# Kernel tuning notes

Hardware: AMD Instinct MI355X
Metric: run time of the kernel (lower is better)

Reference implementation:

```python
import jax, jax.numpy as jnp
import numpy as np

N_LEVELS = 16
F_PER = 2
LOG2_HASH = 19
HASH_MASK = np.uint32(2 ** LOG2_HASH - 1)
BASE_RES = 16.0
FINEST_RES = 512.0
B_GROWTH = float(np.exp((np.log(FINEST_RES) - np.log(BASE_RES)) / (N_LEVELS - 1)))
PI = float(np.pi)
BOX_MIN = np.array([0.0, -PI, 0.5 * PI, -0.85 * PI], dtype=np.float32)
BOX_MAX = np.array([PI, PI, 0.85 * PI, -0.5 * PI], dtype=np.float32)
PRIMES = np.array([1, 2654435761, 805459861, 3674653429], dtype=np.uint32)
OFFSETS = np.array([[i, j, k, l] for i in (0, 1) for j in (0, 1)
                    for k in (0, 1) for l in (0, 1)], dtype=np.int32)  # (16,4)

BATCH = 131072


def setup_inputs() -> dict:
    key = jax.random.key(0)
    ks = jax.random.split(key, 16)
    bmin, bmax = jnp.asarray(BOX_MIN), jnp.asarray(BOX_MAX)
    u = jax.random.uniform(ks[0], (BATCH, 4), dtype=jnp.float32)
    x = bmin + u * (bmax - bmin)  # points inside the box
    tables = jax.random.uniform(ks[1], (N_LEVELS, 2 ** LOG2_HASH, F_PER),
                                minval=-1e-4, maxval=1e-4, dtype=jnp.float32)

    def lin(k, fi, fo):
        s = 1.0 / np.sqrt(fi)
        k1, k2 = jax.random.split(k)
        W = jax.random.uniform(k1, (fi, fo), minval=-s, maxval=s, dtype=jnp.float32)
        b = jax.random.uniform(k2, (fo,), minval=-s, maxval=s, dtype=jnp.float32)
        return W, b

    W1, b1 = lin(ks[2], 5, 512)
    W2, b2 = lin(ks[3], 512, 512)
    W3, b3 = lin(ks[4], 512, 512)
    W4, b4 = lin(ks[5], 512, 512)
    W5, b5 = lin(ks[6], 512, 512)
    W6, b6 = lin(ks[7], 512, 16)
    return dict(x=x, tables=tables, W1=W1, b1=b1, W2=W2, b2=b2, W3=W3, b3=b3,
                W4=W4, b4=b4, W5=W5, b5=b5, W6=W6, b6=b6)


def _forward(x, tables, W1, b1, W2, b2, W3, b3, W4, b4, W5, b5, W6, b6):
    bmin, bmax = jnp.asarray(BOX_MIN), jnp.asarray(BOX_MAX)
    primes = jnp.asarray(PRIMES)            # (4,) uint32
    offsets = jnp.asarray(OFFSETS)          # (16,4) int32
    B = x.shape[0]

    xc = jnp.clip(x, bmin, bmax)
    keep_mask = jnp.all(x == xc, axis=-1)   # (B,)

    resolutions = jnp.floor(BASE_RES * (B_GROWTH ** jnp.arange(N_LEVELS, dtype=jnp.float32)))

    def level_fn(_, lev):
        table, res = lev                     # table: (2^19, 2), res: scalar
        grid = (bmax - bmin) / res           # (4,)
        bl = jnp.floor((xc - bmin) / grid).astype(jnp.int32)      # (B,4) bottom-left voxel
        verts = (bl[:, None, :] + offsets[None]).astype(jnp.uint32)  # (B,16,4)
        h = verts * primes                   # uint32 wraparound multiply
        h = h[..., 0] ^ h[..., 1] ^ h[..., 2] ^ h[..., 3]
        idx = (h & HASH_MASK).astype(jnp.int32)                   # (B,16)
        emb = table[idx]                     # (B,16,2) gather
        # weight MLP on [resolution, x]
        feat = jnp.concatenate([jnp.broadcast_to(res, (B, 1)).astype(x.dtype), x], axis=1)  # (B,5)
        h1 = jax.nn.relu(feat @ W1 + b1)
        h2 = jax.nn.relu(h1 @ W2 + b2)
        h3 = jax.nn.relu(h2 @ W3 + b3)
        h4 = jax.nn.relu(h3 @ W4 + b4)
        h5 = jax.nn.relu(h4 @ W5 + b5)
        w = jax.nn.softmax(h5 @ W6 + b6, axis=1)                  # (B,16)
        out = jnp.einsum('bv,bvf->bf', w, emb)                    # (B,2)
        return None, out

    _, outs = jax.lax.scan(level_fn, None, (tables, resolutions))  # (L,B,2)
    out = jnp.moveaxis(outs, 0, 1).reshape(B, N_LEVELS * F_PER)    # (B,32)
    return out, keep_mask


def reference(x, tables, W1, b1, W2, b2, W3, b3, W4, b4, W5, b5, W6, b6):
    return _forward(x, tables, W1, b1, W2, b2, W3, b3, W4, b4, W5, b5, W6, b6)
```

## Files before the change

### kernel.cpp

```cpp
#include <hip/hip_runtime.h>
#include <stdint.h>

typedef unsigned int uint32;
typedef unsigned short u16;
typedef unsigned char u8;
typedef long long i64;
typedef unsigned long long u64;
typedef __attribute__((ext_vector_type(4))) float f32x4;

#define HASH_BITS 19
#define TABLE_SZ (1u << HASH_BITS)
#define HMASK (TABLE_SZ - 1u)
#define PI_D 3.141592653589793
#define NPTS 131072
#define NWB4 (4 * 512 * 512)

__device__ __forceinline__ u8 f2fp8(float f) {
    int r = __builtin_amdgcn_cvt_pk_fp8_f32(f, f, 0, false);
    return (u8)(r & 0xFF);
}

__device__ const float g_res[16] = {16.f,20.f,25.f,32.f,40.f,50.f,64.f,80.f,
                                    101.f,128.f,161.f,203.f,256.f,322.f,406.f,512.f};

__global__ void prep_weights(const float* __restrict__ W2, const float* __restrict__ W3,
                             const float* __restrict__ W4, const float* __restrict__ W5,
                             u8* __restrict__ wt8) {
    int pid = blockIdx.x * 256 + threadIdx.x;
    int e = pid * 2;
    if (e < NWB4) {
        int m = e >> 18;
        int rem = e & 262143;
        int n = rem >> 9, k = rem & 511;
        const float* W = (m == 0) ? W2 : (m == 1) ? W3 : (m == 2) ? W4 : W5;
        float v0 = W[k * 512 + n], v1 = W[(k + 1) * 512 + n];
        int g = n >> 4, r = n & 15, kk = k >> 5, kg = (k >> 3) & 3;
        int dst = m * 262144 + g * 8192 + kk * 512 + (kg * 16 + r) * 8 + (k & 7);
        int pk = __builtin_amdgcn_cvt_pk_fp8_f32(v0, v1, 0, false);
        *(u16*)(wt8 + dst) = (u16)(pk & 0xFFFF);
    }
}

__global__ void mask_kernel(const float* __restrict__ x, float* __restrict__ mout, int B) {
    int i = blockIdx.x * 256 + threadIdx.x;
    if (i >= B) return;
    constexpr float bmin[4] = {0.0f, (float)(-PI_D), (float)(0.5 * PI_D), (float)(-0.85 * PI_D)};
    constexpr float bmax[4] = {(float)(PI_D), (float)(PI_D), (float)(0.85 * PI_D), (float)(-0.5 * PI_D)};
    float4 v = ((const float4*)x)[i];
    bool ok = (v.x >= bmin[0]) && (v.x <= bmax[0]) &&
              (v.y >= bmin[1]) && (v.y <= bmax[1]) &&
              (v.z >= bmin[2]) && (v.z <= bmax[2]) &&
              (v.w >= bmin[3]) && (v.w <= bmax[3]);
    mout[i] = ok ? 1.0f : 0.0f;
}

__global__ __launch_bounds__(512, 4)
void fused_mlp(const float* __restrict__ x, const float* __restrict__ tables,
               const float* __restrict__ W1, const float* __restrict__ b1,
               const u8* __restrict__ wt8, const float* __restrict__ W6,
               const float* __restrict__ b2, const float* __restrict__ b3,
               const float* __restrict__ b4, const float* __restrict__ b5,
               const float* __restrict__ b6, float* __restrict__ out, int level) {
    __shared__ u8 act[64 * 512];
    __shared__ u8 w1lds[32 * 512];
    __shared__ u8 w6lds[16 * 512];
    __shared__ float xsh[64 * 4];
    __shared__ float swsh[64 * 17];

    const int tid = threadIdx.x;
    const int lane = tid & 63;
    const int wv = tid >> 6;
    const int ptile = blockIdx.x;
    const float res = g_res[level];
    const int lrow = lane & 15;
    const int kg = lane >> 4;

    if (tid < 256) xsh[tid] = x[(size_t)ptile * 256 + tid];
    {
        int base = tid * 32;
#pragma unroll
        for (int i = 0; i < 32; ++i) {
            int d = base + i;
            int g = d >> 9, w = d & 511, l = w >> 3, j = d & 7;
            int n = g * 16 + (l & 15), k = (l >> 4) * 8 + j;
            float v = (k == 0) ? W1[n] * 512.0f : (k <= 4 ? W1[k * 512 + n] : 0.0f);
            w1lds[d] = f2fp8(v);
        }
    }
    {
        int base = tid * 16;
#pragma unroll
        for (int i = 0; i < 16; ++i) {
            int d = base + i;
            int kk = d >> 9, w = d & 511, l = w >> 3, j = d & 7;
            int n = l & 15, k = kk * 32 + (l >> 4) * 8 + j;
            w6lds[d] = f2fp8(W6[k * 16 + n]);
        }
    }
    __syncthreads();

    f32x4 acc[4][4];
#pragma unroll
    for (int rt = 0; rt < 4; ++rt)
#pragma unroll
        for (int ct = 0; ct < 4; ++ct) acc[rt][ct] = (f32x4){0.f, 0.f, 0.f, 0.f};

    {
        float rs = res * (1.0f / 512.0f);
        i64 bfeat[4];
#pragma unroll
        for (int rt = 0; rt < 4; ++rt) {
            float4 xv = *(const float4*)&xsh[(rt * 16 + lrow) * 4];
            uint32 lo = __builtin_amdgcn_cvt_pk_fp8_f32(rs, xv.x, 0, false);
            lo = __builtin_amdgcn_cvt_pk_fp8_f32(xv.y, xv.z, lo, true);
            uint32 hi = __builtin_amdgcn_cvt_pk_fp8_f32(xv.w, 0.0f, 0, false);
            u64 f = ((u64)hi << 32) | lo;
            bfeat[rt] = (kg == 0) ? (i64)f : (i64)0;
        }
#pragma unroll
        for (int ct = 0; ct < 4; ++ct) {
            i64 a1 = *(const i64*)&w1lds[(wv * 4 + ct) * 512 + lane * 8];
#pragma unroll
            for (int rt = 0; rt < 4; ++rt)
                acc[rt][ct] = __builtin_amdgcn_mfma_f32_16x16x32_fp8_fp8(a1, bfeat[rt], acc[rt][ct], 0, 0, 0);
        }
#pragma unroll
        for (int ct = 0; ct < 4; ++ct) {
            int n0 = wv * 64 + ct * 16 + kg * 4;
            float4 bv = *(const float4*)&b1[n0];
            int u = n0 >> 3, lo2 = n0 & 4;
#pragma unroll
            for (int rt = 0; rt < 4; ++rt) {
                int pt = rt * 16 + lrow;
                float v0 = fmaxf(acc[rt][ct][0] + bv.x, 0.f);
                float v1 = fmaxf(acc[rt][ct][1] + bv.y, 0.f);
                float v2 = fmaxf(acc[rt][ct][2] + bv.z, 0.f);
                float v3 = fmaxf(acc[rt][ct][3] + bv.w, 0.f);
                uint32 wrd = __builtin_amdgcn_cvt_pk_fp8_f32(v0, v1, 0, false);
                wrd = __builtin_amdgcn_cvt_pk_fp8_f32(v2, v3, wrd, true);
                *(uint32*)&act[pt * 512 + ((u ^ (pt & 7)) << 3) + lo2] = wrd;
            }
        }
    }
    __syncthreads();

    for (int ly = 0; ly < 4; ++ly) {
        const float* bias = (ly == 0) ? b2 : (ly == 1) ? b3 : (ly == 2) ? b4 : b5;
#pragma unroll
        for (int rt = 0; rt < 4; ++rt)
#pragma unroll
            for (int ct = 0; ct < 4; ++ct) acc[rt][ct] = (f32x4){0.f, 0.f, 0.f, 0.f};

#pragma unroll
        for (int kk = 0; kk < 16; ++kk) {
            i64 aw[4], ba[4];
#pragma unroll
            for (int ct = 0; ct < 4; ++ct)
                aw[ct] = *(const i64*)&wt8[ly * 262144 + (wv * 4 + ct) * 8192 + kk * 512 + lane * 8];
#pragma unroll
            for (int rt = 0; rt < 4; ++rt) {
                int pt = rt * 16 + lrow;
                ba[rt] = *(const i64*)&act[pt * 512 + (((kk * 4 + kg) ^ (pt & 7)) << 3)];
            }
#pragma unroll
            for (int rt = 0; rt < 4; ++rt)
#pragma unroll
                for (int ct = 0; ct < 4; ++ct)
                    acc[rt][ct] = __builtin_amdgcn_mfma_f32_16x16x32_fp8_fp8(aw[ct], ba[rt], acc[rt][ct], 0, 0, 0);
        }
        __syncthreads();
#pragma unroll
        for (int ct = 0; ct < 4; ++ct) {
            int n0 = wv * 64 + ct * 16 + kg * 4;
            float4 bv = *(const float4*)&bias[n0];
            int u = n0 >> 3, lo2 = n0 & 4;
#pragma unroll
            for (int rt = 0; rt < 4; ++rt) {
                int pt = rt * 16 + lrow;
                float v0 = fmaxf(acc[rt][ct][0] + bv.x, 0.f);
                float v1 = fmaxf(acc[rt][ct][1] + bv.y, 0.f);
                float v2 = fmaxf(acc[rt][ct][2] + bv.z, 0.f);
                float v3 = fmaxf(acc[rt][ct][3] + bv.w, 0.f);
                uint32 wrd = __builtin_amdgcn_cvt_pk_fp8_f32(v0, v1, 0, false);
                wrd = __builtin_amdgcn_cvt_pk_fp8_f32(v2, v3, wrd, true);
                *(uint32*)&act[pt * 512 + ((u ^ (pt & 7)) << 3) + lo2] = wrd;
            }
        }
        __syncthreads();
    }

    if (wv < 4) {
        f32x4 a6 = {0.f, 0.f, 0.f, 0.f};
        const int pt = wv * 16 + lrow;
#pragma unroll
        for (int kk = 0; kk < 16; ++kk) {
            i64 aw = *(const i64*)&w6lds[kk * 512 + lane * 8];
            i64 ba = *(const i64*)&act[pt * 512 + (((kk * 4 + kg) ^ (pt & 7)) << 3)];
            a6 = __builtin_amdgcn_mfma_f32_16x16x32_fp8_fp8(aw, ba, a6, 0, 0, 0);
        }
        int n0 = kg * 4;
        float4 bv = *(const float4*)&b6[n0];
        swsh[pt * 17 + n0 + 0] = a6[0] + bv.x;
        swsh[pt * 17 + n0 + 1] = a6[1] + bv.y;
        swsh[pt * 17 + n0 + 2] = a6[2] + bv.z;
        swsh[pt * 17 + n0 + 3] = a6[3] + bv.w;
    }
    __syncthreads();

    if (tid < 64) {
        float zv[16];
        float m = -1e30f;
#pragma unroll
        for (int j = 0; j < 16; ++j) { zv[j] = swsh[tid * 17 + j]; m = fmaxf(m, zv[j]); }
        float s = 0.f;
#pragma unroll
        for (int j = 0; j < 16; ++j) { zv[j] = expf(zv[j] - m); s += zv[j]; }
        float inv = 1.0f / s;
#pragma unroll
        for (int j = 0; j < 16; ++j) swsh[tid * 17 + j] = zv[j] * inv;
    }
    __syncthreads();

    {
        constexpr float bmin[4] = {0.0f, (float)(-PI_D), (float)(0.5 * PI_D), (float)(-0.85 * PI_D)};
        constexpr float bmax[4] = {(float)(PI_D), (float)(PI_D), (float)(0.85 * PI_D), (float)(-0.5 * PI_D)};
        constexpr uint32 primes[4] = {1u, 2654435761u, 805459861u, 3674653429u};
        const int p = tid >> 3;
        const int pr = tid & 7;
        uint32 ca[4], cb[4];
#pragma unroll
        for (int d = 0; d < 4; ++d) {
            float xv = xsh[p * 4 + d];
            float xc = fminf(fmaxf(xv, bmin[d]), bmax[d]);
            float g = (bmax[d] - bmin[d]) / res;
            float t = (xc - bmin[d]) / g;
            int bl = (int)floorf(t);
            ca[d] = (uint32)bl * primes[d];
            cb[d] = (uint32)(bl + 1) * primes[d];
        }
        float s0 = 0.f, s1 = 0.f;
        const float* tb = tables + (size_t)level * TABLE_SZ * 2;
#pragma unroll
        for (int vv = 0; vv < 2; ++vv) {
            int v = pr * 2 + vv;
            uint32 h = ((v & 8) ? cb[0] : ca[0]) ^ ((v & 4) ? cb[1] : ca[1]) ^
                       ((v & 2) ? cb[2] : ca[2]) ^ ((v & 1) ? cb[3] : ca[3]);
            float2 e = *(const float2*)(tb + (size_t)(h & HMASK) * 2);
            float wgt = swsh[p * 17 + v];
            s0 = fmaf(wgt, e.x, s0);
            s1 = fmaf(wgt, e.y, s1);
        }
#pragma unroll
        for (int sft = 1; sft < 8; sft <<= 1) {
            s0 += __shfl_xor(s0, sft, 64);
            s1 += __shfl_xor(s1, sft, 64);
        }
        if (pr == 0) {
            float* o = out + (size_t)(ptile * 64 + p) * 32 + level * 2;
            __builtin_nontemporal_store(s0, o);
            __builtin_nontemporal_store(s1, o + 1);
        }
    }
}

extern "C" void kernel_launch(void* const* d_in, const int* in_sizes, int n_in,
                              void* d_out, int out_size, void* d_ws, size_t ws_size,
                              hipStream_t stream) {
    const float* x      = (const float*)d_in[0];
    const float* tables = (const float*)d_in[1];
    const float* W1 = (const float*)d_in[2];
    const float* b1 = (const float*)d_in[3];
    const float* W2 = (const float*)d_in[4];
    const float* b2 = (const float*)d_in[5];
    const float* W3 = (const float*)d_in[6];
    const float* b3 = (const float*)d_in[7];
    const float* W4 = (const float*)d_in[8];
    const float* b4 = (const float*)d_in[9];
    const float* W5 = (const float*)d_in[10];
    const float* b5 = (const float*)d_in[11];
    const float* W6 = (const float*)d_in[12];
    const float* b6 = (const float*)d_in[13];

    const int B = in_sizes[0] / 4;
    u8* wt8 = (u8*)d_ws;

    prep_weights<<<(NWB4 / 2 + 255) / 256, 256, 0, stream>>>(W2, W3, W4, W5, wt8);

    for (int level = 0; level < 16; ++level) {
        fused_mlp<<<dim3(NPTS / 64), 512, 0, stream>>>(
            x, tables, W1, b1, wt8, W6, b2, b3, b4, b5, b6, (float*)d_out, level);
    }
    mask_kernel<<<(B + 255) / 256, 256, 0, stream>>>(x, (float*)d_out + (size_t)B * 32, B);
}
```

Measured before the change: 3.614 ms.

## Switch MLP matmuls to 32x32x64 scaled FP8 MFMA with relaid weights

Replaces the 16x16x32 fp8 MFMA tiling with the gfx950 32x32x64 f8f6f4 scaled MFMA (unit scales), using 2x2 output tiles of 32 per wave. Weight prep and the activation LDS layout are rearranged into 32-byte K-chunks per lane, so each operand load is 256 bits. The per-element swizzle goes away, and the first layer's weights are built in registers instead of going through LDS. The aim is to issue fewer MFMA instructions and fewer LDS and global loads per FLOP, at the cost of possible LDS bank conflicts from the unswizzled 32-byte-stride layout.

Result: faster. 3.241 ms (-10.3%).

```diff
diff --git a/kernel.cpp b/kernel.cpp
--- a/kernel.cpp
+++ b/kernel.cpp
@@ -4,9 +4,8 @@
 typedef unsigned int uint32;
 typedef unsigned short u16;
 typedef unsigned char u8;
-typedef long long i64;
-typedef unsigned long long u64;
-typedef __attribute__((ext_vector_type(4))) float f32x4;
+typedef __attribute__((ext_vector_type(8))) int i32x8;
+typedef __attribute__((ext_vector_type(16))) float f32x16;
 
 #define HASH_BITS 19
 #define TABLE_SZ (1u << HASH_BITS)
@@ -14,6 +13,9 @@
 #define PI_D 3.141592653589793
 #define NPTS 131072
 #define NWB4 (4 * 512 * 512)
+
+#define MFMA64(A, B, C) __builtin_amdgcn_mfma_scale_f32_32x32x64_f8f6f4( \
+    (A), (B), (C), 0, 0, 0, 0x7F7F7F7F, 0, 0x7F7F7F7F)
 
 __device__ __forceinline__ u8 f2fp8(float f) {
     int r = __builtin_amdgcn_cvt_pk_fp8_f32(f, f, 0, false);
@@ -34,8 +36,8 @@
         int n = rem >> 9, k = rem & 511;
         const float* W = (m == 0) ? W2 : (m == 1) ? W3 : (m == 2) ? W4 : W5;
         float v0 = W[k * 512 + n], v1 = W[(k + 1) * 512 + n];
-        int g = n >> 4, r = n & 15, kk = k >> 5, kg = (k >> 3) & 3;
-        int dst = m * 262144 + g * 8192 + kk * 512 + (kg * 16 + r) * 8 + (k & 7);
+        int g32 = n >> 5, l = (n & 31) + (((k >> 5) & 1) << 5), kk = k >> 6, j = k & 31;
+        int dst = m * 262144 + g32 * 16384 + kk * 2048 + l * 32 + j;
         int pk = __builtin_amdgcn_cvt_pk_fp8_f32(v0, v1, 0, false);
         *(u16*)(wt8 + dst) = (u16)(pk & 0xFFFF);
     }
@@ -61,19 +63,18 @@
                const float* __restrict__ b2, const float* __restrict__ b3,
                const float* __restrict__ b4, const float* __restrict__ b5,
                const float* __restrict__ b6, float* __restrict__ out, int level) {
-    __shared__ u8 act[64 * 512];
-    __shared__ u8 w1lds[32 * 512];
-    __shared__ u8 w6lds[16 * 512];
+    __shared__ u8 act[32768];
+    __shared__ u8 w6lds[16384];
     __shared__ float xsh[64 * 4];
     __shared__ float swsh[64 * 17];
 
     const int tid = threadIdx.x;
     const int lane = tid & 63;
     const int wv = tid >> 6;
+    const int pl = lane & 31;
+    const int kh = lane >> 5;
     const int ptile = blockIdx.x;
     const float res = g_res[level];
-    const int lrow = lane & 15;
-    const int kg = lane >> 4;
 
     if (tid < 256) xsh[tid] = x[(size_t)ptile * 256 + tid];
     {
@@ -81,129 +82,111 @@
 #pragma unroll
         for (int i = 0; i < 32; ++i) {
             int d = base + i;
-            int g = d >> 9, w = d & 511, l = w >> 3, j = d & 7;
-            int n = g * 16 + (l & 15), k = (l >> 4) * 8 + j;
-            float v = (k == 0) ? W1[n] * 512.0f : (k <= 4 ? W1[k * 512 + n] : 0.0f);
-            w1lds[d] = f2fp8(v);
-        }
-    }
+            int kk = d >> 11, l = (d >> 5) & 63, j = d & 31;
+            int n = l & 31, k = kk * 64 + (l >> 5) * 32 + j;
+            w6lds[d] = (n < 16) ? f2fp8(W6[k * 16 + n]) : (u8)0;
+        }
+    }
+    __syncthreads();
+
+    f32x16 acc00, acc01, acc10, acc11;
+
     {
-        int base = tid * 16;
-#pragma unroll
-        for (int i = 0; i < 16; ++i) {
-            int d = base + i;
-            int kk = d >> 9, w = d & 511, l = w >> 3, j = d & 7;
-            int n = l & 15, k = kk * 32 + (l >> 4) * 8 + j;
-            w6lds[d] = f2fp8(W6[k * 16 + n]);
-        }
-    }
-    __syncthreads();
-
-    f32x4 acc[4][4];
-#pragma unroll
-    for (int rt = 0; rt < 4; ++rt)
-#pragma unroll
-        for (int ct = 0; ct < 4; ++ct) acc[rt][ct] = (f32x4){0.f, 0.f, 0.f, 0.f};
-
-    {
+        f32x16 zc = {0.f,0.f,0.f,0.f,0.f,0.f,0.f,0.f,0.f,0.f,0.f,0.f,0.f,0.f,0.f,0.f};
         float rs = res * (1.0f / 512.0f);
-        i64 bfeat[4];
-#pragma unroll
-        for (int rt = 0; rt < 4; ++rt) {
-            float4 xv = *(const float4*)&xsh[(rt * 16 + lrow) * 4];
-            uint32 lo = __builtin_amdgcn_cvt_pk_fp8_f32(rs, xv.x, 0, false);
-            lo = __builtin_amdgcn_cvt_pk_fp8_f32(xv.y, xv.z, lo, true);
-            uint32 hi = __builtin_amdgcn_cvt_pk_fp8_f32(xv.w, 0.0f, 0, false);
-            u64 f = ((u64)hi << 32) | lo;
-            bfeat[rt] = (kg == 0) ? (i64)f : (i64)0;
-        }
-#pragma unroll
-        for (int ct = 0; ct < 4; ++ct) {
-            i64 a1 = *(const i64*)&w1lds[(wv * 4 + ct) * 512 + lane * 8];
-#pragma unroll
-            for (int rt = 0; rt < 4; ++rt)
-                acc[rt][ct] = __builtin_amdgcn_mfma_f32_16x16x32_fp8_fp8(a1, bfeat[rt], acc[rt][ct], 0, 0, 0);
-        }
-#pragma unroll
-        for (int ct = 0; ct < 4; ++ct) {
-            int n0 = wv * 64 + ct * 16 + kg * 4;
-            float4 bv = *(const float4*)&b1[n0];
-            int u = n0 >> 3, lo2 = n0 & 4;
-#pragma unroll
-            for (int rt = 0; rt < 4; ++rt) {
-                int pt = rt * 16 + lrow;
-                float v0 = fmaxf(acc[rt][ct][0] + bv.x, 0.f);
-                float v1 = fmaxf(acc[rt][ct][1] + bv.y, 0.f);
-                float v2 = fmaxf(acc[rt][ct][2] + bv.z, 0.f);
-                float v3 = fmaxf(acc[rt][ct][3] + bv.w, 0.f);
-                uint32 wrd = __builtin_amdgcn_cvt_pk_fp8_f32(v0, v1, 0, false);
-                wrd = __builtin_amdgcn_cvt_pk_fp8_f32(v2, v3, wrd, true);
-                *(uint32*)&act[pt * 512 + ((u ^ (pt & 7)) << 3) + lo2] = wrd;
+        i32x8 a1[2], bf[2];
+#pragma unroll
+        for (int ct = 0; ct < 2; ++ct) {
+            int n = wv * 64 + ct * 32 + pl;
+            uint32 w0 = 0, w1 = 0;
+            if (kh == 0) {
+                w0 = __builtin_amdgcn_cvt_pk_fp8_f32(W1[n] * 512.0f, W1[512 + n], 0, false);
+                w0 = __builtin_amdgcn_cvt_pk_fp8_f32(W1[1024 + n], W1[1536 + n], w0, true);
+                w1 = __builtin_amdgcn_cvt_pk_fp8_f32(W1[2048 + n], 0.0f, 0, false);
             }
-        }
-    }
-    __syncthreads();
-
+            a1[ct] = (i32x8){(int)w0, (int)w1, 0, 0, 0, 0, 0, 0};
+        }
+#pragma unroll
+        for (int rt = 0; rt < 2; ++rt) {
+            float4 xv = *(const float4*)&xsh[(rt * 32 + pl) * 4];
+            uint32 w0 = 0, w1 = 0;
+            if (kh == 0) {
+                w0 = __builtin_amdgcn_cvt_pk_fp8_f32(rs, xv.x, 0, false);
+                w0 = __builtin_amdgcn_cvt_pk_fp8_f32(xv.y, xv.z, w0, true);
+                w1 = __builtin_amdgcn_cvt_pk_fp8_f32(xv.w, 0.0f, 0, false);
+            }
+            bf[rt] = (i32x8){(int)w0, (int)w1, 0, 0, 0, 0, 0, 0};
+        }
+        acc00 = MFMA64(a1[0], bf[0], zc);
+        acc01 = MFMA64(a1[1], bf[0], zc);
+        acc10 = MFMA64(a1[0], bf[1], zc);
+        acc11 = MFMA64(a1[1], bf[1], zc);
+    }
+
+#define EPI(ACC, RT, CT, BIASP) do {                                           \
+        int nb = wv * 64 + (CT) * 32;                                          \
+        _Pragma("unroll")                                                      \
+        for (int q = 0; q < 4; ++q) {                                          \
+            int nn = nb + q * 8 + 4 * kh;                                      \
+            float4 bv = *(const float4*)&(BIASP)[nn];                          \
+            float v0 = fmaxf((ACC)[q * 4 + 0] + bv.x, 0.f);                    \
+            float v1 = fmaxf((ACC)[q * 4 + 1] + bv.y, 0.f);                    \
+            float v2 = fmaxf((ACC)[q * 4 + 2] + bv.z, 0.f);                    \
+            float v3 = fmaxf((ACC)[q * 4 + 3] + bv.w, 0.f);                    \
+            uint32 wrd = __builtin_amdgcn_cvt_pk_fp8_f32(v0, v1, 0, false);    \
+            wrd = __builtin_amdgcn_cvt_pk_fp8_f32(v2, v3, wrd, true);          \
+            *(uint32*)&act[(RT) * 16384 + (wv * 2 + (CT)) * 1024 + pl * 32     \
+                           + q * 8 + 4 * kh] = wrd;                            \
+        }                                                                      \
+    } while (0)
+
+    EPI(acc00, 0, 0, b1); EPI(acc01, 0, 1, b1);
+    EPI(acc10, 1, 0, b1); EPI(acc11, 1, 1, b1);
+    __syncthreads();
+
+#pragma unroll
     for (int ly = 0; ly < 4; ++ly) {
         const float* bias = (ly == 0) ? b2 : (ly == 1) ? b3 : (ly == 2) ? b4 : b5;
-#pragma unroll
-        for (int rt = 0; rt < 4; ++rt)
-#pragma unroll
-            for (int ct = 0; ct < 4; ++ct) acc[rt][ct] = (f32x4){0.f, 0.f, 0.f, 0.f};
-
-#pragma unroll
-        for (int kk = 0; kk < 16; ++kk) {
-            i64 aw[4], ba[4];
-#pragma unroll
-            for (int ct = 0; ct < 4; ++ct)
-                aw[ct] = *(const i64*)&wt8[ly * 262144 + (wv * 4 + ct) * 8192 + kk * 512 + lane * 8];
-#pragma unroll
-            for (int rt = 0; rt < 4; ++rt) {
-                int pt = rt * 16 + lrow;
-                ba[rt] = *(const i64*)&act[pt * 512 + (((kk * 4 + kg) ^ (pt & 7)) << 3)];
-            }
-#pragma unroll
-            for (int rt = 0; rt < 4; ++rt)
-#pragma unroll
-                for (int ct = 0; ct < 4; ++ct)
-                    acc[rt][ct] = __builtin_amdgcn_mfma_f32_16x16x32_fp8_fp8(aw[ct], ba[rt], acc[rt][ct], 0, 0, 0);
-        }
+        const u8* lyb = wt8 + ly * 262144 + wv * 32768;
+        f32x16 n00 = {0.f,0.f,0.f,0.f,0.f,0.f,0.f,0.f,0.f,0.f,0.f,0.f,0.f,0.f,0.f,0.f};
+        f32x16 n01 = n00, n10 = n00, n11 = n00;
+#pragma unroll
+        for (int kk = 0; kk < 8; ++kk) {
+            int koff = (kk * 2 + kh) * 1024 + pl * 32;
+            i32x8 ba0 = *(const i32x8*)&act[koff];
+            i32x8 ba1 = *(const i32x8*)&act[16384 + koff];
+            i32x8 aw0 = *(const i32x8*)&lyb[kk * 2048 + lane * 32];
+            i32x8 aw1 = *(const i32x8*)&lyb[16384 + kk * 2048 + lane * 32];
+            n00 = MFMA64(aw0, ba0, n00);
+            n10 = MFMA64(aw0, ba1, n10);
+            n01 = MFMA64(aw1, ba0, n01);
+            n11 = MFMA64(aw1, ba1, n11);
+        }
+        acc00 = n00; acc01 = n01; acc10 = n10; acc11 = n11;
         __syncthreads();
-#pragma unroll
-        for (int ct = 0; ct < 4; ++ct) {
-            int n0 = wv * 64 + ct * 16 + kg * 4;
-            float4 bv = *(const float4*)&bias[n0];
-            int u = n0 >> 3, lo2 = n0 & 4;
-#pragma unroll
-            for (int rt = 0; rt < 4; ++rt) {
-                int pt = rt * 16 + lrow;
-                float v0 = fmaxf(acc[rt][ct][0] + bv.x, 0.f);
-                float v1 = fmaxf(acc[rt][ct][1] + bv.y, 0.f);
-                float v2 = fmaxf(acc[rt][ct][2] + bv.z, 0.f);
-                float v3 = fmaxf(acc[rt][ct][3] + bv.w, 0.f);
-                uint32 wrd = __builtin_amdgcn_cvt_pk_fp8_f32(v0, v1, 0, false);
-                wrd = __builtin_amdgcn_cvt_pk_fp8_f32(v2, v3, wrd, true);
-                *(uint32*)&act[pt * 512 + ((u ^ (pt & 7)) << 3) + lo2] = wrd;
-            }
-        }
+        EPI(acc00, 0, 0, bias); EPI(acc01, 0, 1, bias);
+        EPI(acc10, 1, 0, bias); EPI(acc11, 1, 1, bias);
         __syncthreads();
     }
 
-    if (wv < 4) {
-        f32x4 a6 = {0.f, 0.f, 0.f, 0.f};
-        const int pt = wv * 16 + lrow;
-#pragma unroll
-        for (int kk = 0; kk < 16; ++kk) {
-            i64 aw = *(const i64*)&w6lds[kk * 512 + lane * 8];
-            i64 ba = *(const i64*)&act[pt * 512 + (((kk * 4 + kg) ^ (pt & 7)) << 3)];
-            a6 = __builtin_amdgcn_mfma_f32_16x16x32_fp8_fp8(aw, ba, a6, 0, 0, 0);
-        }
-        int n0 = kg * 4;
-        float4 bv = *(const float4*)&b6[n0];
-        swsh[pt * 17 + n0 + 0] = a6[0] + bv.x;
-        swsh[pt * 17 + n0 + 1] = a6[1] + bv.y;
-        swsh[pt * 17 + n0 + 2] = a6[2] + bv.z;
-        swsh[pt * 17 + n0 + 3] = a6[3] + bv.w;
+    if (wv < 2) {
+        f32x16 a6 = {0.f,0.f,0.f,0.f,0.f,0.f,0.f,0.f,0.f,0.f,0.f,0.f,0.f,0.f,0.f,0.f};
+#pragma unroll
+        for (int kk = 0; kk < 8; ++kk) {
+            i32x8 aw = *(const i32x8*)&w6lds[kk * 2048 + lane * 32];
+            i32x8 ba = *(const i32x8*)&act[wv * 16384 + (kk * 2 + kh) * 1024 + pl * 32];
+            a6 = MFMA64(aw, ba, a6);
+        }
+        int pt = wv * 32 + pl;
+#pragma unroll
+        for (int q = 0; q < 2; ++q) {
+            int n0 = q * 8 + 4 * kh;
+            float4 bv = *(const float4*)&b6[n0];
+            swsh[pt * 17 + n0 + 0] = a6[q * 4 + 0] + bv.x;
+            swsh[pt * 17 + n0 + 1] = a6[q * 4 + 1] + bv.y;
+            swsh[pt * 17 + n0 + 2] = a6[q * 4 + 2] + bv.z;
+            swsh[pt * 17 + n0 + 3] = a6[q * 4 + 3] + bv.w;
+        }
     }
     __syncthreads();
 
@@ -261,6 +244,7 @@
             __builtin_nontemporal_store(s1, o + 1);
         }
     }
+#undef EPI
 }
 
 extern "C" void kernel_launch(void* const* d_in, const int* in_sizes, int n_in,
```
